# Kernel optimization log

Measured on AMD Instinct MI355X. Metric: run time of the kernel, lower is better.

Reference implementation:

```python
import jax, jax.numpy as jnp
import numpy as np

DIM = 192
HEADS = 8
B, H, W = 8, 128, 128

def _dwconv3x3(x, w):
    # x: [B,C,H,W], w: [C,1,3,3] depthwise
    return jax.lax.conv_general_dilated(
        x, w, window_strides=(1, 1), padding=((1, 1), (1, 1)),
        dimension_numbers=('NCHW', 'OIHW', 'NCHW'),
        feature_group_count=x.shape[1])

def _proj(x, pw, dw):
    # 1x1 pointwise (as einsum) followed by 3x3 depthwise
    y = jnp.einsum('bchw,oc->bohw', x, pw)
    return _dwconv3x3(y, dw)

def setup_inputs() -> dict:
    key = jax.random.key(0)
    ks = jax.random.split(key, 9)
    s_pw = 1.0 / np.sqrt(DIM)
    s_dw = 1.0 / 3.0
    return {
        'x_feat': jax.random.normal(ks[0], (B, DIM, H, W), jnp.float32),
        'y_feat': jax.random.normal(ks[1], (B, DIM, H, W), jnp.float32),
        'q_pw': jax.random.normal(ks[2], (DIM, DIM), jnp.float32) * s_pw,
        'q_dw': jax.random.normal(ks[3], (DIM, 1, 3, 3), jnp.float32) * s_dw,
        'k_pw': jax.random.normal(ks[4], (DIM, DIM), jnp.float32) * s_pw,
        'k_dw': jax.random.normal(ks[5], (DIM, 1, 3, 3), jnp.float32) * s_dw,
        'v_pw': jax.random.normal(ks[6], (DIM, DIM), jnp.float32) * s_pw,
        'v_dw': jax.random.normal(ks[7], (DIM, 1, 3, 3), jnp.float32) * s_dw,
        'proj_w': jax.random.normal(ks[8], (DIM, DIM), jnp.float32) * s_pw,
        'temperature': jnp.ones((HEADS, 1, 1), jnp.float32),
    }

def reference(x_feat, y_feat, q_pw, q_dw, k_pw, k_dw, v_pw, v_dw, proj_w, temperature):
    b, c, h, w = x_feat.shape
    ch = c // HEADS  # channels per head
    q = _proj(x_feat, q_pw, q_dw)
    k = _proj(y_feat, k_pw, k_dw)
    v = _proj(y_feat, v_pw, v_dw)
    # b (head c) h w -> b head c (h w)
    to_heads = lambda t: t.reshape(b, HEADS, ch, h * w)
    q, k, v = to_heads(q), to_heads(k), to_heads(v)
    # L2-normalize along token dim (torch F.normalize eps=1e-12)
    q = q / jnp.maximum(jnp.linalg.norm(q, axis=-1, keepdims=True), 1e-12)
    k = k / jnp.maximum(jnp.linalg.norm(k, axis=-1, keepdims=True), 1e-12)
    attn = jnp.einsum('bhcn,bhdn->bhcd', q, k) * temperature  # [b,heads,ch,ch]
    attn = jax.nn.softmax(attn, axis=-1)
    out = jnp.einsum('bhcd,bhdn->bhcn', attn, v)
    out = out.reshape(b, c, h, w)
    out = jnp.einsum('bchw,oc->bohw', out, proj_w)
    return out
```

## Files before the change

### kernel.cpp

```cpp
#include <hip/hip_runtime.h>
#include <hip/hip_bf16.h>

#define BATCH 8
#define CDIM 192
#define HEADS 8
#define CH 24
#define HH 128
#define WW 128
#define NPIX (HH*WW)
#define NELEM (BATCH*CDIM*NPIX)
#define NP4 (NPIX/4)

#define NSLAB 32
#define NJOBS 624

typedef __attribute__((ext_vector_type(8))) short bf16x8;
typedef __attribute__((ext_vector_type(4))) float f32x4;
typedef __attribute__((ext_vector_type(4))) unsigned int u32x4;

#define UNIT 100663296ull
__device__ __align__(256) unsigned char g_pool[4 * UNIT + (16u << 20)];

#define OFF_T0   (0 * UNIT)
#define OFF_Q    (1 * UNIT)
#define OFF_K    (2 * UNIT)
#define OFF_V    (3 * UNIT)
#define OFF_MISC (4 * UNIT)
#define OFF_PART (OFF_MISC)
#define OFF_S    (OFF_MISC + 5111808ull)
#define OFF_M    (OFF_S + 159744ull)
#define OFF_MF   (OFF_M + 1179648ull)

__device__ inline unsigned short bf_rne(float x) {
  unsigned u = __float_as_uint(x);
  unsigned r = (u + 0x7fffu + ((u >> 16) & 1u)) >> 16;
  return (unsigned short)r;
}
__device__ inline void f32_split(float x, unsigned short& h, unsigned short& l) {
  h = bf_rne(x);
  float hf = __uint_as_float(((unsigned)h) << 16);
  l = bf_rne(x - hf);
}

__global__ __launch_bounds__(64) void w_to_frag(const float* __restrict__ W,
                                                unsigned short* __restrict__ F,
                                                int nb) {
  const int b = blockIdx.x / 12, mf = blockIdx.x % 12;
  const int lane = threadIdx.x;
  const int row = mf * 16 + (lane & 15);
  const size_t lo = (size_t)nb * CDIM * CDIM;
#pragma unroll
  for (int ks = 0; ks < 6; ++ks) {
    const int k0 = ks * 32 + (lane >> 4) * 8;
    const float* src = W + ((size_t)b * CDIM + row) * CDIM + k0;
    bf16x8 hv, lv;
#pragma unroll
    for (int j = 0; j < 8; ++j) {
      unsigned short h, l;
      f32_split(src[j], h, l);
      hv[j] = (short)h;
      lv[j] = (short)l;
    }
    const size_t didx = (((size_t)(blockIdx.x) * 6 + ks) * 64 + lane) * 8;
    *(bf16x8*)(F + didx) = hv;
    *(bf16x8*)(F + lo + didx) = lv;
  }
}

__global__ __launch_bounds__(256, 2) void mfma_gemm192(
    const float* __restrict__ X,
    const unsigned short* __restrict__ WF, size_t w_lo,
    int w_bstride,
    float* __restrict__ Out) {
  const int bn = blockIdx.x;
  const int b = blockIdx.y;
  const int t = threadIdx.x;
  const int lane = t & 63, wid = t >> 6;
  const int wm = wid >> 1, wn = wid & 1;
  const int kq = lane >> 4;

  __shared__ float Xs[32][132];

  const size_t wbase = (size_t)b * w_bstride;
  const float* Xb = X + (size_t)b * CDIM * NPIX;
  const int col4 = (t & 31) * 4;
  const int r0 = t >> 5;
  const int pxl = wn * 64 + (lane & 15);

  f32x4 acc[6][4];
#pragma unroll
  for (int mi = 0; mi < 6; ++mi)
#pragma unroll
    for (int ni = 0; ni < 4; ++ni) acc[mi][ni] = (f32x4){0.f, 0.f, 0.f, 0.f};

  for (int ks = 0; ks < 6; ++ks) {
    float4 st[4];
#pragma unroll
    for (int p = 0; p < 4; ++p)
      st[p] = *(const float4*)(Xb + (size_t)(ks * 32 + r0 + 8 * p) * NPIX +
                               bn * 128 + col4);
#pragma unroll
    for (int p = 0; p < 4; ++p)
      *(float4*)&Xs[r0 + 8 * p][col4 ^ ((p & 1) << 4)] = st[p];
    __syncthreads();

    bf16x8 Ah[6], Al[6];
#pragma unroll
    for (int mi = 0; mi < 6; ++mi) {
      const int mf = wm * 6 + mi;
      const size_t idx = wbase + (((size_t)(mf * 6 + ks)) * 64 + lane) * 8;
      Ah[mi] = *(const bf16x8*)(WF + idx);
      Al[mi] = *(const bf16x8*)(WF + w_lo + idx);
    }

    u32x4 Bh[4], Bl[4];
#pragma unroll
    for (int ni = 0; ni < 4; ++ni) {
      const int pxs = (pxl + ni * 16) ^ ((kq & 1) << 4);
#pragma unroll
      for (int jp = 0; jp < 4; ++jp) {
        const float x0 = Xs[kq * 8 + 2 * jp][pxs];
        const float x1 = Xs[kq * 8 + 2 * jp + 1][pxs];
        const unsigned u0 = __float_as_uint(x0);
        const unsigned u1 = __float_as_uint(x1);
        Bh[ni][jp] = (u1 & 0xffff0000u) | (u0 >> 16);
        const float rr0 = x0 - __uint_as_float(u0 & 0xffff0000u);
        const float rr1 = x1 - __uint_as_float(u1 & 0xffff0000u);
        Bl[ni][jp] = ((unsigned)bf_rne(rr1) << 16) | (unsigned)bf_rne(rr0);
      }
    }
    __syncthreads();

#pragma unroll
    for (int mi = 0; mi < 6; ++mi)
#pragma unroll
      for (int ni = 0; ni < 4; ++ni) {
        const bf16x8 bh = __builtin_bit_cast(bf16x8, Bh[ni]);
        const bf16x8 bl = __builtin_bit_cast(bf16x8, Bl[ni]);
        acc[mi][ni] = __builtin_amdgcn_mfma_f32_16x16x32_bf16(
            Ah[mi], bh, acc[mi][ni], 0, 0, 0);
        acc[mi][ni] = __builtin_amdgcn_mfma_f32_16x16x32_bf16(
            Ah[mi], bl, acc[mi][ni], 0, 0, 0);
        acc[mi][ni] = __builtin_amdgcn_mfma_f32_16x16x32_bf16(
            Al[mi], bh, acc[mi][ni], 0, 0, 0);
      }
  }

  const int ocol = bn * 128 + wn * 64 + (lane & 15);
  const int orow = wm * 96 + (lane >> 4) * 4;
#pragma unroll
  for (int mi = 0; mi < 6; ++mi)
#pragma unroll
    for (int r = 0; r < 4; ++r) {
      const int och = orow + mi * 16 + r;
      float* dst = Out + ((size_t)b * CDIM + och) * NPIX + ocol;
#pragma unroll
      for (int ni = 0; ni < 4; ++ni) dst[ni * 16] = acc[mi][ni][r];
    }
}

__global__ __launch_bounds__(256) void dwconv(const float* __restrict__ In,
                                              const float* __restrict__ Wd,
                                              float* __restrict__ Out) {
  const int idx = blockIdx.x * 256 + threadIdx.x;
  if (idx >= NELEM / 4) return;
  const int x4 = (idx & 31) * 4;
  const int y = (idx >> 5) & 127;
  const int c = (idx >> 12) % CDIM;
  const int b = idx / (32 * 128 * CDIM);

  const float* base = In + (size_t)(b * CDIM + c) * NPIX;
  float w[9];
#pragma unroll
  for (int i = 0; i < 9; ++i) w[i] = Wd[c * 9 + i];

  float acc0 = 0.f, acc1 = 0.f, acc2 = 0.f, acc3 = 0.f;
#pragma unroll
  for (int dy = 0; dy < 3; ++dy) {
    const int yy = y + dy - 1;
    if (yy < 0 || yy > 127) continue;
    const float* row = base + yy * WW;
    float vb0 = (x4 > 0) ? row[x4 - 1] : 0.f;
    const float4 m = *(const float4*)(row + x4);
    const float vb5 = (x4 + 4 < WW) ? row[x4 + 4] : 0.f;
    const float w0 = w[dy * 3 + 0], w1 = w[dy * 3 + 1], w2 = w[dy * 3 + 2];
    acc0 += w0 * vb0 + w1 * m.x + w2 * m.y;
    acc1 += w0 * m.x + w1 * m.y + w2 * m.z;
    acc2 += w0 * m.y + w1 * m.z + w2 * m.w;
    acc3 += w0 * m.z + w1 * m.w + w2 * vb5;
  }
  float4 o;
  o.x = acc0; o.y = acc1; o.z = acc2; o.w = acc3;
  *(float4*)(Out + (size_t)idx * 4) = o;
}

__global__ __launch_bounds__(256) void dots_partial(const float* __restrict__ Q,
                                                    const float* __restrict__ K,
                                                    float* __restrict__ Part) {
  const int bh = blockIdx.x;
  const int slab = blockIdx.y;
  const int b = bh >> 3, h = bh & 7;
  const int t = threadIdx.x;
  const int pg = t & 15;
  const int sb = t >> 4;
  const int sr = sb >> 2, sc = sb & 3;
  const bool diag = (sr == sc);

  const float4* qb = (const float4*)(Q + (size_t)(b * CDIM + h * CH) * NPIX);
  const float4* kb = (const float4*)(K + (size_t)(b * CDIM + h * CH) * NPIX);
  const int F_PER_SLAB = NP4 / NSLAB;
  const int NITER = F_PER_SLAB / 16;

  float acc[6][6];
#pragma unroll
  for (int j = 0; j < 6; ++j)
#pragma unroll
    for (int c = 0; c < 6; ++c) acc[j][c] = 0.f;
  float qq[6] = {0, 0, 0, 0, 0, 0};
  float kk[6] = {0, 0, 0, 0, 0, 0};

  const int f0 = slab * F_PER_SLAB + pg;
  for (int i = 0; i < NITER; ++i) {
    const int f = f0 + 16 * i;
    float4 qv[6], kv[6];
#pragma unroll
    for (int j = 0; j < 6; ++j) qv[j] = qb[(size_t)(sr * 6 + j) * NP4 + f];
#pragma unroll
    for (int j = 0; j < 6; ++j) kv[j] = kb[(size_t)(sc * 6 + j) * NP4 + f];
#pragma unroll
    for (int j = 0; j < 6; ++j)
#pragma unroll
      for (int c = 0; c < 6; ++c)
        acc[j][c] += qv[j].x * kv[c].x + qv[j].y * kv[c].y +
                     qv[j].z * kv[c].z + qv[j].w * kv[c].w;
    if (diag) {
#pragma unroll
      for (int j = 0; j < 6; ++j) {
        qq[j] += qv[j].x * qv[j].x + qv[j].y * qv[j].y + qv[j].z * qv[j].z +
                 qv[j].w * qv[j].w;
        kk[j] += kv[j].x * kv[j].x + kv[j].y * kv[j].y + kv[j].z * kv[j].z +
                 kv[j].w * kv[j].w;
      }
    }
  }

#pragma unroll
  for (int j = 0; j < 6; ++j)
#pragma unroll
    for (int c = 0; c < 6; ++c) {
      float v = acc[j][c];
      v += __shfl_xor(v, 1);
      v += __shfl_xor(v, 2);
      v += __shfl_xor(v, 4);
      v += __shfl_xor(v, 8);
      acc[j][c] = v;
    }
#pragma unroll
  for (int j = 0; j < 6; ++j) {
    float a = qq[j], bb = kk[j];
    a += __shfl_xor(a, 1); a += __shfl_xor(a, 2);
    a += __shfl_xor(a, 4); a += __shfl_xor(a, 8);
    bb += __shfl_xor(bb, 1); bb += __shfl_xor(bb, 2);
    bb += __shfl_xor(bb, 4); bb += __shfl_xor(bb, 8);
    qq[j] = a; kk[j] = bb;
  }

  if (pg == 0) {
    float* P = Part + ((size_t)bh * NSLAB + slab) * NJOBS;
#pragma unroll
    for (int j = 0; j < 6; ++j)
#pragma unroll
      for (int c = 0; c < 6; ++c)
        P[(sr * 6 + j) * 24 + sc * 6 + c] = acc[j][c];
    if (diag) {
#pragma unroll
      for (int j = 0; j < 6; ++j) {
        P[576 + sr * 6 + j] = qq[j];
        P[600 + sc * 6 + j] = kk[j];
      }
    }
  }
}

__global__ __launch_bounds__(640) void dots_reduce(const float* __restrict__ Part,
                                                   float* __restrict__ S) {
  const int bh = blockIdx.x;
  const int job = threadIdx.x;
  if (job >= NJOBS) return;
  float s = 0.f;
  for (int i = 0; i < NSLAB; ++i)
    s += Part[((size_t)bh * NSLAB + i) * NJOBS + job];
  S[bh * NJOBS + job] = s;
}

__global__ __launch_bounds__(576) void build_M(const float* __restrict__ S,
                                               const float* __restrict__ PW,
                                               const float* __restrict__ Temp,
                                               float* __restrict__ M) {
  const int b = blockIdx.x, h = blockIdx.y;
  const int bh = b * 8 + h;
  __shared__ float att[CH][CH];
  __shared__ float qn[CH], kn[CH];
  const int t = threadIdx.x;
  const float* Sb = S + (size_t)bh * NJOBS;

  if (t < CH) {
    qn[t] = fmaxf(sqrtf(Sb[576 + t]), 1e-12f);
    kn[t] = fmaxf(sqrtf(Sb[600 + t]), 1e-12f);
  }
  __syncthreads();
  const float temp = Temp[h];
  if (t < 576) {
    const int c = t / 24, d = t % 24;
    att[c][d] = Sb[t] / (qn[c] * kn[d]) * temp;
  }
  __syncthreads();
  if (t < CH) {
    float mx = -1e30f;
    for (int d = 0; d < CH; ++d) mx = fmaxf(mx, att[t][d]);
    float sum = 0.f;
    for (int d = 0; d < CH; ++d) {
      const float e = __expf(att[t][d] - mx);
      att[t][d] = e;
      sum += e;
    }
    const float inv = 1.f / sum;
    for (int d = 0; d < CH; ++d) att[t][d] *= inv;
  }
  __syncthreads();
  for (int i = t; i < CDIM * CH; i += 576) {
    const int o = i / CH, d = i % CH;
    float s = 0.f;
#pragma unroll
    for (int c = 0; c < CH; ++c) s += PW[o * CDIM + h * CH + c] * att[c][d];
    M[((size_t)b * CDIM + o) * CDIM + h * CH + d] = s;
  }
}


extern "C" void kernel_launch(void* const* d_in, const int* in_sizes, int n_in,
                              void* d_out, int out_size, void* d_ws, size_t ws_size,
                              hipStream_t stream) {
  const float* x_feat = (const float*)d_in[0];
  const float* y_feat = (const float*)d_in[1];
  const float* q_pw   = (const float*)d_in[2];
  const float* q_dw   = (const float*)d_in[3];
  const float* k_pw   = (const float*)d_in[4];
  const float* k_dw   = (const float*)d_in[5];
  const float* v_pw   = (const float*)d_in[6];
  const float* v_dw   = (const float*)d_in[7];
  const float* proj_w = (const float*)d_in[8];
  const float* temp   = (const float*)d_in[9];
  float* out = (float*)d_out;

  unsigned char* pool;
  (void)hipGetSymbolAddress((void**)&pool, HIP_SYMBOL(g_pool));
  float* t0 = (float*)(pool + OFF_T0);
  float* q  = (float*)(pool + OFF_Q);
  float* k  = (float*)(pool + OFF_K);
  float* v  = (float*)(pool + OFF_V);
  float* part = (float*)(pool + OFF_PART);
  float* S    = (float*)(pool + OFF_S);
  float* M    = (float*)(pool + OFF_M);
  unsigned short* MF = (unsigned short*)(pool + OFF_MF);

  unsigned short* WQF = MF + 2ull * 8 * CDIM * CDIM;
  unsigned short* WKF = WQF + 2ull * CDIM * CDIM;
  unsigned short* WVF = WKF + 2ull * CDIM * CDIM;

  const size_t w1_lo = (size_t)1 * CDIM * CDIM;
  const size_t w8_lo = (size_t)8 * CDIM * CDIM;

  const dim3 ggrid(NPIX / 128, BATCH);
  const int dwgrid = (NELEM / 4) / 256;

  w_to_frag<<<12, 64, 0, stream>>>(q_pw, WQF, 1);
  w_to_frag<<<12, 64, 0, stream>>>(k_pw, WKF, 1);
  w_to_frag<<<12, 64, 0, stream>>>(v_pw, WVF, 1);

  mfma_gemm192<<<ggrid, 256, 0, stream>>>(x_feat, WQF, w1_lo, 0, t0);
  dwconv<<<dwgrid, 256, 0, stream>>>(t0, q_dw, q);
  mfma_gemm192<<<ggrid, 256, 0, stream>>>(y_feat, WKF, w1_lo, 0, t0);
  dwconv<<<dwgrid, 256, 0, stream>>>(t0, k_dw, k);
  mfma_gemm192<<<ggrid, 256, 0, stream>>>(y_feat, WVF, w1_lo, 0, t0);
  dwconv<<<dwgrid, 256, 0, stream>>>(t0, v_dw, v);

  dots_partial<<<dim3(64, NSLAB), 256, 0, stream>>>(q, k, part);
  dots_reduce<<<64, 640, 0, stream>>>(part, S);
  build_M<<<dim3(BATCH, HEADS), 576, 0, stream>>>(S, proj_w, temp, M);
  w_to_frag<<<8 * 12, 64, 0, stream>>>(M, MF, 8);

  mfma_gemm192<<<ggrid, 256, 0, stream>>>(v, MF, w8_lo, CDIM * CDIM, out);
}
```

Baseline: 433.7 us.

## Double-buffer GEMM LDS via direct global-to-LDS loads and batch depthwise convs

The pointwise GEMM now stages X tiles into a double-buffered LDS array with global_load_lds, prefetching the next K slab while the current one is converted and fed to MFMA. This drops one barrier per iteration and removes register staging. The three depthwise convolutions are merged into a single launch by giving each projection its own intermediate buffer. That needs two extra 96MB scratch buffers and adds per-block pointer selection, and the swizzle layout also changed, which may alter LDS bank conflicts.

```diff
diff --git a/kernel.cpp b/kernel.cpp
--- a/kernel.cpp
+++ b/kernel.cpp
@@ -17,15 +17,20 @@
 typedef __attribute__((ext_vector_type(8))) short bf16x8;
 typedef __attribute__((ext_vector_type(4))) float f32x4;
 typedef __attribute__((ext_vector_type(4))) unsigned int u32x4;
+typedef unsigned int u32;
+typedef const __attribute__((address_space(1))) u32* gas_ptr;
+typedef __attribute__((address_space(3))) u32* las_ptr;
 
 #define UNIT 100663296ull
-__device__ __align__(256) unsigned char g_pool[4 * UNIT + (16u << 20)];
-
-#define OFF_T0   (0 * UNIT)
-#define OFF_Q    (1 * UNIT)
-#define OFF_K    (2 * UNIT)
-#define OFF_V    (3 * UNIT)
-#define OFF_MISC (4 * UNIT)
+__device__ __align__(256) unsigned char g_pool[6 * UNIT + (16u << 20)];
+
+#define OFF_T0Q  (0 * UNIT)
+#define OFF_T0K  (1 * UNIT)
+#define OFF_T0V  (2 * UNIT)
+#define OFF_Q    (3 * UNIT)
+#define OFF_K    (4 * UNIT)
+#define OFF_V    (5 * UNIT)
+#define OFF_MISC (6 * UNIT)
 #define OFF_PART (OFF_MISC)
 #define OFF_S    (OFF_MISC + 5111808ull)
 #define OFF_M    (OFF_S + 159744ull)
@@ -79,30 +84,46 @@
   const int wm = wid >> 1, wn = wid & 1;
   const int kq = lane >> 4;
 
-  __shared__ float Xs[32][132];
+  __shared__ float Xs[2][32][128];
 
   const size_t wbase = (size_t)b * w_bstride;
-  const float* Xb = X + (size_t)b * CDIM * NPIX;
-  const int col4 = (t & 31) * 4;
-  const int r0 = t >> 5;
+  const float* Xb = X + (size_t)b * CDIM * NPIX + bn * 128;
   const int pxl = wn * 64 + (lane & 15);
 
+  int srow[4], scol4[4];
+#pragma unroll
+  for (int p = 0; p < 4; ++p) {
+    const int f = (wid * 4 + p) * 64 + lane;
+    srow[p] = f >> 5;
+    scol4[p] = (f & 31) ^ (((srow[p] >> 3) & 1) << 2);
+  }
+
   f32x4 acc[6][4];
 #pragma unroll
   for (int mi = 0; mi < 6; ++mi)
 #pragma unroll
     for (int ni = 0; ni < 4; ++ni) acc[mi][ni] = (f32x4){0.f, 0.f, 0.f, 0.f};
 
+#pragma unroll
+  for (int p = 0; p < 4; ++p) {
+    const float* src = Xb + (size_t)(srow[p]) * NPIX + scol4[p] * 4;
+    las_ptr dst = (las_ptr)(void*)(&Xs[0][0][0] + (wid * 4 + p) * 256);
+    __builtin_amdgcn_global_load_lds((gas_ptr)(const void*)src, dst, 16, 0, 0);
+  }
+  __syncthreads();
+
+  int cur = 0;
   for (int ks = 0; ks < 6; ++ks) {
-    float4 st[4];
-#pragma unroll
-    for (int p = 0; p < 4; ++p)
-      st[p] = *(const float4*)(Xb + (size_t)(ks * 32 + r0 + 8 * p) * NPIX +
-                               bn * 128 + col4);
-#pragma unroll
-    for (int p = 0; p < 4; ++p)
-      *(float4*)&Xs[r0 + 8 * p][col4 ^ ((p & 1) << 4)] = st[p];
-    __syncthreads();
+    if (ks < 5) {
+#pragma unroll
+      for (int p = 0; p < 4; ++p) {
+        const float* src =
+            Xb + (size_t)((ks + 1) * 32 + srow[p]) * NPIX + scol4[p] * 4;
+        las_ptr dst =
+            (las_ptr)(void*)(&Xs[cur ^ 1][0][0] + (wid * 4 + p) * 256);
+        __builtin_amdgcn_global_load_lds((gas_ptr)(const void*)src, dst, 16, 0, 0);
+      }
+    }
 
     bf16x8 Ah[6], Al[6];
 #pragma unroll
@@ -119,8 +140,8 @@
       const int pxs = (pxl + ni * 16) ^ ((kq & 1) << 4);
 #pragma unroll
       for (int jp = 0; jp < 4; ++jp) {
-        const float x0 = Xs[kq * 8 + 2 * jp][pxs];
-        const float x1 = Xs[kq * 8 + 2 * jp + 1][pxs];
+        const float x0 = Xs[cur][kq * 8 + 2 * jp][pxs];
+        const float x1 = Xs[cur][kq * 8 + 2 * jp + 1][pxs];
         const unsigned u0 = __float_as_uint(x0);
         const unsigned u1 = __float_as_uint(x1);
         Bh[ni][jp] = (u1 & 0xffff0000u) | (u0 >> 16);
@@ -129,7 +150,6 @@
         Bl[ni][jp] = ((unsigned)bf_rne(rr1) << 16) | (unsigned)bf_rne(rr0);
       }
     }
-    __syncthreads();
 
 #pragma unroll
     for (int mi = 0; mi < 6; ++mi)
@@ -144,6 +164,9 @@
         acc[mi][ni] = __builtin_amdgcn_mfma_f32_16x16x32_bf16(
             Al[mi], bh, acc[mi][ni], 0, 0, 0);
       }
+
+    __syncthreads();
+    cur ^= 1;
   }
 
   const int ocol = bn * 128 + wn * 64 + (lane & 15);
@@ -159,11 +182,19 @@
     }
 }
 
-__global__ __launch_bounds__(256) void dwconv(const float* __restrict__ In,
-                                              const float* __restrict__ Wd,
-                                              float* __restrict__ Out) {
-  const int idx = blockIdx.x * 256 + threadIdx.x;
-  if (idx >= NELEM / 4) return;
+#define DWBLK ((NELEM / 4) / 256)
+
+__global__ __launch_bounds__(256) void dwconv3(
+    const float* __restrict__ T0Q, const float* __restrict__ T0K,
+    const float* __restrict__ T0V, const float* __restrict__ QDW,
+    const float* __restrict__ KDW, const float* __restrict__ VDW,
+    float* __restrict__ Q, float* __restrict__ K, float* __restrict__ V) {
+  const int ts = blockIdx.x / DWBLK;
+  const int idx = (blockIdx.x - ts * DWBLK) * 256 + threadIdx.x;
+  const float* In = (ts == 0) ? T0Q : (ts == 1) ? T0K : T0V;
+  const float* Wd = (ts == 0) ? QDW : (ts == 1) ? KDW : VDW;
+  float* Out = (ts == 0) ? Q : (ts == 1) ? K : V;
+
   const int x4 = (idx & 31) * 4;
   const int y = (idx >> 5) & 127;
   const int c = (idx >> 12) % CDIM;
@@ -355,7 +386,9 @@
 
   unsigned char* pool;
   (void)hipGetSymbolAddress((void**)&pool, HIP_SYMBOL(g_pool));
-  float* t0 = (float*)(pool + OFF_T0);
+  float* t0q = (float*)(pool + OFF_T0Q);
+  float* t0k = (float*)(pool + OFF_T0K);
+  float* t0v = (float*)(pool + OFF_T0V);
   float* q  = (float*)(pool + OFF_Q);
   float* k  = (float*)(pool + OFF_K);
   float* v  = (float*)(pool + OFF_V);
@@ -372,18 +405,17 @@
   const size_t w8_lo = (size_t)8 * CDIM * CDIM;
 
   const dim3 ggrid(NPIX / 128, BATCH);
-  const int dwgrid = (NELEM / 4) / 256;
 
   w_to_frag<<<12, 64, 0, stream>>>(q_pw, WQF, 1);
   w_to_frag<<<12, 64, 0, stream>>>(k_pw, WKF, 1);
   w_to_frag<<<12, 64, 0, stream>>>(v_pw, WVF, 1);
 
-  mfma_gemm192<<<ggrid, 256, 0, stream>>>(x_feat, WQF, w1_lo, 0, t0);
-  dwconv<<<dwgrid, 256, 0, stream>>>(t0, q_dw, q);
-  mfma_gemm192<<<ggrid, 256, 0, stream>>>(y_feat, WKF, w1_lo, 0, t0);
-  dwconv<<<dwgrid, 256, 0, stream>>>(t0, k_dw, k);
-  mfma_gemm192<<<ggrid, 256, 0, stream>>>(y_feat, WVF, w1_lo, 0, t0);
-  dwconv<<<dwgrid, 256, 0, stream>>>(t0, v_dw, v);
+  mfma_gemm192<<<ggrid, 256, 0, stream>>>(x_feat, WQF, w1_lo, 0, t0q);
+  mfma_gemm192<<<ggrid, 256, 0, stream>>>(y_feat, WKF, w1_lo, 0, t0k);
+  mfma_gemm192<<<ggrid, 256, 0, stream>>>(y_feat, WVF, w1_lo, 0, t0v);
+
+  dwconv3<<<3 * DWBLK, 256, 0, stream>>>(t0q, t0k, t0v, q_dw, k_dw, v_dw,
+                                         q, k, v);
 
   dots_partial<<<dim3(64, NSLAB), 256, 0, stream>>>(q, k, part);
   dots_reduce<<<64, 640, 0, stream>>>(part, S);
```

Measured after the change: 479.8 us. 1.11x slower.
